# Optimization experiments

Measured on AMD Instinct MI355X. Metric: run time of the kernel, lower is better.

The kernel has to match this reference:

```python
import jax, jax.numpy as jnp
import numpy as np

H = W = 256
CX = CY = 128
N_RINGS = 16
RING_W = 8


def _ring_indices():
    """Static per-ring pixel coordinate lists (cv2 filled-circle rasterization
    approximated by Euclidean distance: ring i = { inner_r < dist <= outer_r }).
    Ring 0 excludes the exact center pixel, matching cv2.circle(radius=0) erase."""
    yy, xx = np.mgrid[0:H, 0:W]
    dist = np.sqrt((xx - CX) ** 2 + (yy - CY) ** 2)
    rings = []
    for i in range(N_RINGS):
        m = (dist <= (i + 1) * RING_W) & (dist > i * RING_W)
        ys, xs = np.nonzero(m)
        rings.append((jnp.asarray(ys), jnp.asarray(xs)))
    return rings

_RINGS = _ring_indices()


def setup_inputs() -> dict:
    key = jax.random.key(0)
    # normalized image in [0,1) so denorm->uint8 quantization never wraps
    image_tensor = jax.random.uniform(key, (256, 3, 256, 256), dtype=jnp.float32)
    return {"image_tensor": image_tensor}


def reference(image_tensor):
    # denormalize and quantize exactly like (img*0.5+0.5)*255 -> uint8 (truncation)
    img = jnp.floor((image_tensor * 0.5 + 0.5) * 255.0)  # [B,3,H,W], values 0..255
    feats = []
    for ys, xs in _RINGS:  # fixed 16-iteration structural loop
        px = img[:, :, ys, xs]                # [B, 3, N_ring] gather
        mean = jnp.mean(px, axis=-1)          # [B, 3]
        std = jnp.std(px, axis=-1)            # population std (ddof=0) like np
        med = jnp.median(px, axis=-1)         # [B, 3]
        feats.append(jnp.concatenate([mean, std, med], axis=-1))  # [B, 9]
    return jnp.stack(feats, axis=1)  # [B, 16, 9]
```

## Files before the change

### kernel.cpp

```cpp
#include <hip/hip_runtime.h>

#define IH 256
#define IW 256
#define NRINGS 16
#define HW_BRC 128
#define HW_B   (NRINGS * 3 * HW_BRC)
#define HW_TOT (256 * HW_B)
#define HW_BYTES ((size_t)HW_TOT * 4)

__global__ __launch_bounds__(256)
void k0_zero(uint4* __restrict__ h) {
    h[blockIdx.x * 256 + threadIdx.x] = make_uint4(0u, 0u, 0u, 0u);
}

__global__ __launch_bounds__(256)
void k1_hist(const float* __restrict__ img, unsigned int* __restrict__ gh) {
    const int b   = blockIdx.x;
    const int s   = blockIdx.y;
    const int tid = threadIdx.x;

    __shared__ unsigned int hist[NRINGS * 3 * HW_BRC];

    for (int i = tid; i < NRINGS * 3 * HW_BRC; i += 256) hist[i] = 0u;
    __syncthreads();

    const int xg  = (tid & 63) * 4;
    const int ry0 = tid >> 6;
    const float* base = img + (size_t)b * 3 * IH * IW;

    const int dx0 = xg - 128;
    int dxs[4];
    #pragma unroll
    for (int j = 0; j < 4; ++j) dxs[j] = (dx0 + j) * (dx0 + j);
    int admin = (dx0 <= 0 && dx0 + 3 >= 0) ? 0 : min(abs(dx0), abs(dx0 + 3));
    const int admin2 = admin * admin;

    for (int ry = ry0; ry < 32; ry += 4) {
        const int y   = (s << 5) + ry;
        const int dy  = y - 128;
        const int dy2 = dy * dy;
        if (dy2 + admin2 > 16384) continue;

        const int off = y * IW + xg;
        const float4 f0 = *(const float4*)(base + off);
        const float4 f1 = *(const float4*)(base + IH * IW + off);
        const float4 f2 = *(const float4*)(base + 2 * IH * IW + off);
        const float va[3][4] = {{f0.x, f0.y, f0.z, f0.w},
                                {f1.x, f1.y, f1.z, f1.w},
                                {f2.x, f2.y, f2.z, f2.w}};

        #pragma unroll
        for (int j = 0; j < 4; ++j) {
            const int d2 = dy2 + dxs[j];
            if (d2 == 0 || d2 > 16384) continue;
            int k = (int)ceilf(sqrtf((float)d2) * 0.125f);
            if (64 * k * k < d2) k++;
            else if (k > 1 && 64 * (k - 1) * (k - 1) >= d2) k--;
            const int ring = k - 1;
            #pragma unroll
            for (int c = 0; c < 3; ++c) {
                const float f = va[c][j];
                int iv = (int)floorf((f * 0.5f + 0.5f) * 255.0f);
                iv = min(max(iv, 0), 255);
                atomicAdd(&hist[(ring * 3 + c) * HW_BRC + (iv >> 1)],
                          1u << ((iv & 1) << 4));
            }
        }
    }

    __syncthreads();
    unsigned int* gb = gh + (size_t)b * HW_B;
    for (int i = tid; i < HW_B; i += 256) {
        const unsigned int v = hist[i];
        if (v) atomicAdd(&gb[i], v);
    }
}

__global__ __launch_bounds__(64)
void k2_stats(const unsigned int* __restrict__ gh, float* __restrict__ out) {
    const int b    = blockIdx.x;
    const int ring = blockIdx.y;
    const int c    = threadIdx.x;
    if (c >= 3) return;

    const unsigned int* h = gh + (size_t)b * HW_B + (ring * 3 + c) * HW_BRC;

    unsigned int n = 0, sum = 0, sumsq = 0;
    #pragma unroll 8
    for (int w = 0; w < HW_BRC; ++w) {
        const unsigned int v  = h[w];
        const unsigned int c0 = v & 0xffffu;
        const unsigned int c1 = v >> 16;
        const unsigned int v0 = 2 * w, v1 = 2 * w + 1;
        n     += c0 + c1;
        sum   += c0 * v0 + c1 * v1;
        sumsq += c0 * v0 * v0 + c1 * v1 * v1;
    }

    const double dn   = (double)n;
    const double mean = (double)sum / dn;
    double var = (double)sumsq / dn - mean * mean;
    if (var < 0.0) var = 0.0;

    const unsigned int j1 = (n - 1u) >> 1;
    const unsigned int j2 = n >> 1;
    unsigned int cum = 0;
    int v1i = -1, v2i = -1;
    for (int w = 0; w < HW_BRC; ++w) {
        const unsigned int v = h[w];
        cum += v & 0xffffu;
        if (v1i < 0 && cum > j1) v1i = 2 * w;
        if (v2i < 0 && cum > j2) { v2i = 2 * w; break; }
        cum += v >> 16;
        if (v1i < 0 && cum > j1) v1i = 2 * w + 1;
        if (v2i < 0 && cum > j2) { v2i = 2 * w + 1; break; }
    }

    float* o = out + ((size_t)b * NRINGS + ring) * 9;
    o[c]     = (float)mean;
    o[3 + c] = (float)sqrt(var);
    o[6 + c] = 0.5f * (float)(v1i + v2i);
}

__global__ __launch_bounds__(256)
void radial_ring_feats(const float* __restrict__ img, float* __restrict__ out) {
    const int b = blockIdx.x, ring = blockIdx.y, tid = threadIdx.x;
    const int Rout = 8 * (ring + 1), Rin = 8 * ring;
    const int R2out = Rout * Rout, R2in = Rin * Rin;
    const int side = 2 * Rout + 1, total = side * side;
    __shared__ unsigned int hist[3][256];
    __shared__ unsigned int s_sum[3], s_sq[3], s_cnt;
    #pragma unroll
    for (int i = 0; i < 3; ++i) hist[i][tid] = 0u;
    if (tid < 3) { s_sum[tid] = 0u; s_sq[tid] = 0u; }
    if (tid == 0) s_cnt = 0u;
    __syncthreads();
    unsigned int ls[3] = {0,0,0}, lq[3] = {0,0,0}, lcnt = 0;
    const float* base = img + (size_t)b * 3 * IH * IW;
    for (int idx = tid; idx < total; idx += 256) {
        const int dy = idx / side - Rout, dx = idx % side - Rout;
        const int y = 128 + dy, x = 128 + dx, d2 = dx * dx + dy * dy;
        if ((unsigned)y < IH && (unsigned)x < IW && d2 <= R2out && d2 > R2in) {
            const int off = y * IW + x;
            #pragma unroll
            for (int c = 0; c < 3; ++c) {
                float f = base[c * IH * IW + off];
                int iv = (int)floorf((f * 0.5f + 0.5f) * 255.0f);
                iv = min(max(iv, 0), 255);
                atomicAdd(&hist[c][iv], 1u);
                ls[c] += (unsigned)iv; lq[c] += (unsigned)(iv * iv);
            }
            lcnt++;
        }
    }
    #pragma unroll
    for (int o = 32; o > 0; o >>= 1) {
        #pragma unroll
        for (int c = 0; c < 3; ++c) {
            ls[c] += (unsigned)__shfl_down((int)ls[c], o, 64);
            lq[c] += (unsigned)__shfl_down((int)lq[c], o, 64);
        }
        lcnt += (unsigned)__shfl_down((int)lcnt, o, 64);
    }
    if ((tid & 63) == 0) {
        #pragma unroll
        for (int c = 0; c < 3; ++c) { atomicAdd(&s_sum[c], ls[c]); atomicAdd(&s_sq[c], lq[c]); }
        atomicAdd(&s_cnt, lcnt);
    }
    __syncthreads();
    if (tid < 3) {
        const int c = tid;
        const unsigned int n = s_cnt;
        const double mean = (double)s_sum[c] / (double)n;
        double var = (double)s_sq[c] / (double)n - mean * mean;
        if (var < 0.0) var = 0.0;
        const unsigned int j1 = (n - 1u) >> 1, j2 = n >> 1;
        unsigned int cum = 0; int v1 = -1, v2 = -1;
        for (int v = 0; v < 256; ++v) {
            cum += hist[c][v];
            if (v1 < 0 && cum > j1) v1 = v;
            if (cum > j2) { v2 = v; break; }
        }
        float* o = out + ((size_t)b * NRINGS + ring) * 9;
        o[c] = (float)mean; o[3 + c] = (float)sqrt(var); o[6 + c] = 0.5f * (float)(v1 + v2);
    }
}

extern "C" void kernel_launch(void* const* d_in, const int* in_sizes, int n_in,
                              void* d_out, int out_size, void* d_ws, size_t ws_size,
                              hipStream_t stream) {
    const float* img = (const float*)d_in[0];
    float* out = (float*)d_out;
    if (ws_size >= HW_BYTES) {
        unsigned int* gh = (unsigned int*)d_ws;
        k0_zero<<<HW_TOT / 4 / 256, 256, 0, stream>>>((uint4*)gh);
        k1_hist<<<dim3(256, 8), 256, 0, stream>>>(img, gh);
        k2_stats<<<dim3(256, NRINGS), 64, 0, stream>>>(gh, out);
    } else {
        radial_ring_feats<<<dim3(256, NRINGS), 256, 0, stream>>>(img, out);
    }
}
```

Baseline: 312.1 us.

## Fuse zero, histogram and stats kernels into one per-image block

Replaces the three-kernel pipeline (global histogram zeroing, per-slab shared histograms merged into global memory with atomics, then a stats kernel) with a single kernel. One 1024-thread block per image builds the full packed histogram in shared memory, then 48 threads compute the mean, std and median directly from it. This removes two launches, the global workspace traffic and the global atomics. In exchange the grid drops to 256 large blocks, which lowers parallelism and leaves a serial tail where only 48 threads work.

```diff
diff --git a/kernel.cpp b/kernel.cpp
--- a/kernel.cpp
+++ b/kernel.cpp
@@ -4,39 +4,30 @@
 #define IW 256
 #define NRINGS 16
 #define HW_BRC 128
-#define HW_B   (NRINGS * 3 * HW_BRC)
-#define HW_TOT (256 * HW_B)
-#define HW_BYTES ((size_t)HW_TOT * 4)
 
-__global__ __launch_bounds__(256)
-void k0_zero(uint4* __restrict__ h) {
-    h[blockIdx.x * 256 + threadIdx.x] = make_uint4(0u, 0u, 0u, 0u);
-}
-
-__global__ __launch_bounds__(256)
-void k1_hist(const float* __restrict__ img, unsigned int* __restrict__ gh) {
+__global__ __launch_bounds__(1024)
+void radial_fused(const float* __restrict__ img, float* __restrict__ out) {
     const int b   = blockIdx.x;
-    const int s   = blockIdx.y;
     const int tid = threadIdx.x;
 
     __shared__ unsigned int hist[NRINGS * 3 * HW_BRC];
 
-    for (int i = tid; i < NRINGS * 3 * HW_BRC; i += 256) hist[i] = 0u;
+    for (int i = tid; i < NRINGS * 3 * HW_BRC; i += 1024) hist[i] = 0u;
     __syncthreads();
 
-    const int xg  = (tid & 63) * 4;
-    const int ry0 = tid >> 6;
+    const int xg = (tid & 63) * 4;
+    const int r0 = tid >> 6;
     const float* base = img + (size_t)b * 3 * IH * IW;
 
     const int dx0 = xg - 128;
     int dxs[4];
     #pragma unroll
     for (int j = 0; j < 4; ++j) dxs[j] = (dx0 + j) * (dx0 + j);
-    int admin = (dx0 <= 0 && dx0 + 3 >= 0) ? 0 : min(abs(dx0), abs(dx0 + 3));
+    const int admin  = (dx0 <= 0 && dx0 + 3 >= 0) ? 0 : min(abs(dx0), abs(dx0 + 3));
     const int admin2 = admin * admin;
 
-    for (int ry = ry0; ry < 32; ry += 4) {
-        const int y   = (s << 5) + ry;
+    for (int k = 0; k < 16; ++k) {
+        const int y   = r0 + (k << 4);
         const int dy  = y - 128;
         const int dy2 = dy * dy;
         if (dy2 + admin2 > 16384) continue;
@@ -53,10 +44,10 @@
         for (int j = 0; j < 4; ++j) {
             const int d2 = dy2 + dxs[j];
             if (d2 == 0 || d2 > 16384) continue;
-            int k = (int)ceilf(sqrtf((float)d2) * 0.125f);
-            if (64 * k * k < d2) k++;
-            else if (k > 1 && 64 * (k - 1) * (k - 1) >= d2) k--;
-            const int ring = k - 1;
+            int kk = (int)ceilf(sqrtf((float)d2) * 0.125f);
+            if (64 * kk * kk < d2) kk++;
+            else if (kk > 1 && 64 * (kk - 1) * (kk - 1) >= d2) kk--;
+            const int ring = kk - 1;
             #pragma unroll
             for (int c = 0; c < 3; ++c) {
                 const float f = va[c][j];
@@ -69,120 +60,47 @@
     }
 
     __syncthreads();
-    unsigned int* gb = gh + (size_t)b * HW_B;
-    for (int i = tid; i < HW_B; i += 256) {
-        const unsigned int v = hist[i];
-        if (v) atomicAdd(&gb[i], v);
-    }
-}
 
-__global__ __launch_bounds__(64)
-void k2_stats(const unsigned int* __restrict__ gh, float* __restrict__ out) {
-    const int b    = blockIdx.x;
-    const int ring = blockIdx.y;
-    const int c    = threadIdx.x;
-    if (c >= 3) return;
+    if (tid < NRINGS * 3) {
+        const int ring = tid / 3;
+        const int c    = tid - ring * 3;
+        const unsigned int* h = &hist[(ring * 3 + c) * HW_BRC];
 
-    const unsigned int* h = gh + (size_t)b * HW_B + (ring * 3 + c) * HW_BRC;
+        unsigned int n = 0, sum = 0, sumsq = 0;
+        #pragma unroll 8
+        for (int w = 0; w < HW_BRC; ++w) {
+            const unsigned int v  = h[w];
+            const unsigned int c0 = v & 0xffffu;
+            const unsigned int c1 = v >> 16;
+            const unsigned int v0 = 2 * w, v1 = 2 * w + 1;
+            n     += c0 + c1;
+            sum   += c0 * v0 + c1 * v1;
+            sumsq += c0 * v0 * v0 + c1 * v1 * v1;
+        }
 
-    unsigned int n = 0, sum = 0, sumsq = 0;
-    #pragma unroll 8
-    for (int w = 0; w < HW_BRC; ++w) {
-        const unsigned int v  = h[w];
-        const unsigned int c0 = v & 0xffffu;
-        const unsigned int c1 = v >> 16;
-        const unsigned int v0 = 2 * w, v1 = 2 * w + 1;
-        n     += c0 + c1;
-        sum   += c0 * v0 + c1 * v1;
-        sumsq += c0 * v0 * v0 + c1 * v1 * v1;
-    }
+        const double dn   = (double)n;
+        const double mean = (double)sum / dn;
+        double var = (double)sumsq / dn - mean * mean;
+        if (var < 0.0) var = 0.0;
 
-    const double dn   = (double)n;
-    const double mean = (double)sum / dn;
-    double var = (double)sumsq / dn - mean * mean;
-    if (var < 0.0) var = 0.0;
+        const unsigned int j1 = (n - 1u) >> 1;
+        const unsigned int j2 = n >> 1;
+        unsigned int cum = 0;
+        int v1i = -1, v2i = -1;
+        for (int w = 0; w < HW_BRC; ++w) {
+            const unsigned int v = h[w];
+            cum += v & 0xffffu;
+            if (v1i < 0 && cum > j1) v1i = 2 * w;
+            if (v2i < 0 && cum > j2) { v2i = 2 * w; break; }
+            cum += v >> 16;
+            if (v1i < 0 && cum > j1) v1i = 2 * w + 1;
+            if (v2i < 0 && cum > j2) { v2i = 2 * w + 1; break; }
+        }
 
-    const unsigned int j1 = (n - 1u) >> 1;
-    const unsigned int j2 = n >> 1;
-    unsigned int cum = 0;
-    int v1i = -1, v2i = -1;
-    for (int w = 0; w < HW_BRC; ++w) {
-        const unsigned int v = h[w];
-        cum += v & 0xffffu;
-        if (v1i < 0 && cum > j1) v1i = 2 * w;
-        if (v2i < 0 && cum > j2) { v2i = 2 * w; break; }
-        cum += v >> 16;
-        if (v1i < 0 && cum > j1) v1i = 2 * w + 1;
-        if (v2i < 0 && cum > j2) { v2i = 2 * w + 1; break; }
-    }
-
-    float* o = out + ((size_t)b * NRINGS + ring) * 9;
-    o[c]     = (float)mean;
-    o[3 + c] = (float)sqrt(var);
-    o[6 + c] = 0.5f * (float)(v1i + v2i);
-}
-
-__global__ __launch_bounds__(256)
-void radial_ring_feats(const float* __restrict__ img, float* __restrict__ out) {
-    const int b = blockIdx.x, ring = blockIdx.y, tid = threadIdx.x;
-    const int Rout = 8 * (ring + 1), Rin = 8 * ring;
-    const int R2out = Rout * Rout, R2in = Rin * Rin;
-    const int side = 2 * Rout + 1, total = side * side;
-    __shared__ unsigned int hist[3][256];
-    __shared__ unsigned int s_sum[3], s_sq[3], s_cnt;
-    #pragma unroll
-    for (int i = 0; i < 3; ++i) hist[i][tid] = 0u;
-    if (tid < 3) { s_sum[tid] = 0u; s_sq[tid] = 0u; }
-    if (tid == 0) s_cnt = 0u;
-    __syncthreads();
-    unsigned int ls[3] = {0,0,0}, lq[3] = {0,0,0}, lcnt = 0;
-    const float* base = img + (size_t)b * 3 * IH * IW;
-    for (int idx = tid; idx < total; idx += 256) {
-        const int dy = idx / side - Rout, dx = idx % side - Rout;
-        const int y = 128 + dy, x = 128 + dx, d2 = dx * dx + dy * dy;
-        if ((unsigned)y < IH && (unsigned)x < IW && d2 <= R2out && d2 > R2in) {
-            const int off = y * IW + x;
-            #pragma unroll
-            for (int c = 0; c < 3; ++c) {
-                float f = base[c * IH * IW + off];
-                int iv = (int)floorf((f * 0.5f + 0.5f) * 255.0f);
-                iv = min(max(iv, 0), 255);
-                atomicAdd(&hist[c][iv], 1u);
-                ls[c] += (unsigned)iv; lq[c] += (unsigned)(iv * iv);
-            }
-            lcnt++;
-        }
-    }
-    #pragma unroll
-    for (int o = 32; o > 0; o >>= 1) {
-        #pragma unroll
-        for (int c = 0; c < 3; ++c) {
-            ls[c] += (unsigned)__shfl_down((int)ls[c], o, 64);
-            lq[c] += (unsigned)__shfl_down((int)lq[c], o, 64);
-        }
-        lcnt += (unsigned)__shfl_down((int)lcnt, o, 64);
-    }
-    if ((tid & 63) == 0) {
-        #pragma unroll
-        for (int c = 0; c < 3; ++c) { atomicAdd(&s_sum[c], ls[c]); atomicAdd(&s_sq[c], lq[c]); }
-        atomicAdd(&s_cnt, lcnt);
-    }
-    __syncthreads();
-    if (tid < 3) {
-        const int c = tid;
-        const unsigned int n = s_cnt;
-        const double mean = (double)s_sum[c] / (double)n;
-        double var = (double)s_sq[c] / (double)n - mean * mean;
-        if (var < 0.0) var = 0.0;
-        const unsigned int j1 = (n - 1u) >> 1, j2 = n >> 1;
-        unsigned int cum = 0; int v1 = -1, v2 = -1;
-        for (int v = 0; v < 256; ++v) {
-            cum += hist[c][v];
-            if (v1 < 0 && cum > j1) v1 = v;
-            if (cum > j2) { v2 = v; break; }
-        }
         float* o = out + ((size_t)b * NRINGS + ring) * 9;
-        o[c] = (float)mean; o[3 + c] = (float)sqrt(var); o[6 + c] = 0.5f * (float)(v1 + v2);
+        o[c]     = (float)mean;
+        o[3 + c] = (float)sqrt(var);
+        o[6 + c] = 0.5f * (float)(v1i + v2i);
     }
 }
 
@@ -191,12 +109,5 @@
                               hipStream_t stream) {
     const float* img = (const float*)d_in[0];
     float* out = (float*)d_out;
-    if (ws_size >= HW_BYTES) {
-        unsigned int* gh = (unsigned int*)d_ws;
-        k0_zero<<<HW_TOT / 4 / 256, 256, 0, stream>>>((uint4*)gh);
-        k1_hist<<<dim3(256, 8), 256, 0, stream>>>(img, gh);
-        k2_stats<<<dim3(256, NRINGS), 64, 0, stream>>>(gh, out);
-    } else {
-        radial_ring_feats<<<dim3(256, NRINGS), 256, 0, stream>>>(img, out);
-    }
+    radial_fused<<<256, 1024, 0, stream>>>(img, out);
 }
```

New measurement: 284.9 us. 8.7% less time.
